# Kernel tuning notes

Hardware: AMD Instinct MI355X
Metric: run time of the kernel (lower is better)

The kernel has to match this reference:

```python
import jax, jax.numpy as jnp
import numpy as np
from jax import lax

N_FRAMES = 256

def _conv(x, w, b):
    # NCHW conv, stride 3 on mel axis (matches MOSNet CNN that collapses mels 81->27->9->3->1)
    y = lax.conv_general_dilated(x, w, window_strides=(1, 3),
                                 padding=((1, 1), (1, 1)),
                                 dimension_numbers=('NCHW', 'OIHW', 'NCHW'))
    return jax.nn.relu(y + b[None, :, None, None])

def _lstm(x, Wih, Whh, bih, bhh, reverse=False):
    # x: [T, B, D] -> hs: [T, B, H]; PyTorch gate order i, f, g, o
    Bsz, H = x.shape[1], Whh.shape[1]
    bias = bih + bhh
    def step(carry, xt):
        h, c = carry
        z = xt @ Wih.T + h @ Whh.T + bias
        i, f, g, o = jnp.split(z, 4, axis=-1)
        c = jax.nn.sigmoid(f) * c + jax.nn.sigmoid(i) * jnp.tanh(g)
        h = jax.nn.sigmoid(o) * jnp.tanh(c)
        return (h, c), h
    init = (jnp.zeros((Bsz, H), x.dtype), jnp.zeros((Bsz, H), x.dtype))
    _, hs = lax.scan(step, init, x, reverse=reverse)
    return hs

def setup_inputs():
    key = jax.random.key(0)
    ks = jax.random.split(key, 24)
    B, T, M = 16, 4096, 81
    chans = [1, 16, 32, 64, 128]
    H = 128
    FC_IN = 2 * H * N_FRAMES  # 65536
    FC_H = 128
    s = 0.05
    inp = {'audio': jax.random.normal(ks[0], (B, T, M), jnp.float32),
           'sample_lengths': jnp.full((B,), T, dtype=jnp.int32)}
    for li in range(4):
        inp['w%d' % li] = jax.random.normal(ks[1 + 2 * li], (chans[li + 1], chans[li], 3, 3), jnp.float32) * s
        inp['b%d' % li] = jnp.zeros((chans[li + 1],), jnp.float32)
    D = chans[-1]
    for d, off in (('f', 9), ('b', 13)):
        inp['Wih_' + d] = jax.random.normal(ks[off], (4 * H, D), jnp.float32) * s
        inp['Whh_' + d] = jax.random.normal(ks[off + 1], (4 * H, H), jnp.float32) * s
        inp['bih_' + d] = jnp.zeros((4 * H,), jnp.float32)
        inp['bhh_' + d] = jnp.zeros((4 * H,), jnp.float32)
    inp['fc1_w'] = jax.random.normal(ks[17], (FC_H, FC_IN), jnp.float32) * 0.005
    inp['fc1_b'] = jnp.zeros((FC_H,), jnp.float32)
    inp['fs_w'] = jax.random.normal(ks[18], (1, FC_H), jnp.float32) * s
    inp['fs_b'] = jnp.zeros((1,), jnp.float32)
    return inp

def reference(audio, w0, b0, w1, b1, w2, b2, w3, b3,
              Wih_f, Whh_f, bih_f, bhh_f, Wih_b, Whh_b, bih_b, bhh_b,
              fc1_w, fc1_b, fs_w, fs_b, sample_lengths):
    B, T, M = audio.shape
    F = T // N_FRAMES  # all lengths == T, multiple of N_FRAMES -> all frames full
    x = audio.reshape(B * F, 1, N_FRAMES, M)   # [BF, 1, nf, mels]
    for w, b in ((w0, b0), (w1, b1), (w2, b2), (w3, b3)):
        x = _conv(x, w, b)                      # mel axis 81->27->9->3->1
    x = x[..., 0].transpose(2, 0, 1)            # [nf, BF, C]
    h_f = _lstm(x, Wih_f, Whh_f, bih_f, bhh_f)
    h_b = _lstm(x, Wih_b, Whh_b, bih_b, bhh_b, reverse=True)
    h = jnp.concatenate([h_f, h_b], axis=-1).transpose(1, 0, 2)  # [BF, nf, 2H]
    flat = h.reshape(B * F, -1)                 # time-major flatten, matches view(1,-1)
    z = jax.nn.relu(flat @ fc1_w.T + fc1_b)     # dropout is identity at inference
    score = jax.nn.sigmoid(z @ fs_w.T + fs_b) * 4.0 + 1.0  # mos range [1,5]
    frames = score.reshape(B, F)
    utt = frames.mean(axis=1)
    return utt, frames
```

## Files before the change

### kernel.cpp

```cpp
#include <hip/hip_runtime.h>
#include <hip/hip_fp16.h>

#define BF 256
#define TSTEPS 256

typedef _Float16 h8_t __attribute__((ext_vector_type(8)));
typedef _Float16 h4_t __attribute__((ext_vector_type(4)));
typedef float f4_t __attribute__((ext_vector_type(4)));

union H8 { uint4 u; h8_t v; };
union H4 { uint2 u; h4_t v; };
union U2H4 { uint2 u; __half h[4]; };

static __device__ __forceinline__ float sigmoidf_(float x) {
    return __builtin_amdgcn_rcpf(1.f + __expf(-x));
}
static __device__ __forceinline__ float tanhf_(float x) {
    return 1.f - 2.f * __builtin_amdgcn_rcpf(__expf(2.f * x) + 1.f);
}

static __device__ __forceinline__ float xswap32(float x, int lane) {
    typedef unsigned uv2 __attribute__((ext_vector_type(2)));
    unsigned xu = __float_as_uint(x);
    uv2 r = __builtin_amdgcn_permlane32_swap(xu, xu, false, false);
    return __uint_as_float((lane & 32) ? r[0] : r[1]);
}

static __device__ __forceinline__ void wg_barrier_lds() {
    __builtin_amdgcn_sched_barrier(0);
    asm volatile("s_waitcnt lgkmcnt(0)" ::: "memory");
    __builtin_amdgcn_s_barrier();
    __builtin_amdgcn_sched_barrier(0);
}

static __device__ __forceinline__ void pack_one(const float* __restrict__ src,
                                                __half* __restrict__ dst,
                                                int OC, int IC, int KS,
                                                int oc_str, int ic_str, int k_str, int i) {
    int grp = KS / 4;
    int j = i % grp;
    int oc = (i / grp) % OC;
    int g = (i / (grp * OC)) & 3;
    int chunk = i / (grp * OC * 4);
    int CPK = IC / KS;
    int cc = chunk % CPK;
    int khw = chunk / CPK;
    int ic = cc * KS + g * grp + j;
    dst[i] = __float2half(src[(long)oc * oc_str + (long)ic * ic_str + khw * k_str]);
}

static __device__ __forceinline__ void pack_whh_one(const float* __restrict__ src,
                                                    __half* __restrict__ dst, int i) {
    int j = i & 7;
    int prow = (i >> 3) & 511;
    int cg = i >> 12;
    int g = cg & 3, chunk = cg >> 2;
    int t = prow >> 4, rr = prow & 15;
    int cls = rr >> 2, du = rr & 3;
    int orig = cls * 128 + t * 4 + du;
    int ic = chunk * 32 + g * 8 + j;
    dst[i] = __float2half(src[orig * 128 + ic]);
}

__global__ __launch_bounds__(256) void prep_k(
        const float* __restrict__ w0, const float* __restrict__ w1,
        const float* __restrict__ w2, const float* __restrict__ w3,
        const float* __restrict__ Wihf, const float* __restrict__ Wihb,
        const float* __restrict__ Whhf, const float* __restrict__ Whhb,
        float* __restrict__ w0t, __half* __restrict__ w1p,
        __half* __restrict__ w2p, __half* __restrict__ w3p,
        __half* __restrict__ wfp, __half* __restrict__ wbp,
        __half* __restrict__ whhfp, __half* __restrict__ whhbp) {
    int i = blockIdx.x * 256 + threadIdx.x;
    if (i < 144) { int oc = i / 9, rem = i % 9; w0t[rem * 16 + oc] = w0[i]; return; }
    i -= 144;
    if (i < 4608) { pack_one(w1, w1p, 32, 16, 16, 144, 9, 1, i); return; }
    i -= 4608;
    if (i < 18432) { pack_one(w2, w2p, 64, 32, 32, 288, 9, 1, i); return; }
    i -= 18432;
    if (i < 73728) { pack_one(w3, w3p, 128, 64, 32, 576, 9, 1, i); return; }
    i -= 73728;
    if (i < 65536) { pack_one(Wihf, wfp, 512, 128, 32, 128, 1, 0, i); return; }
    i -= 65536;
    if (i < 65536) { pack_one(Wihb, wbp, 512, 128, 32, 128, 1, 0, i); return; }
    i -= 65536;
    if (i < 65536) { pack_whh_one(Whhf, whhfp, i); return; }
    i -= 65536;
    if (i < 65536) { pack_whh_one(Whhb, whhbp, i); return; }
}

__global__ void pack_wf16(const float* __restrict__ src, __half* __restrict__ dst,
                          int OC, int IC, int KS,
                          int oc_str, int ic_str, int k_str, int total) {
    int i = blockIdx.x * 256 + threadIdx.x;
    if (i >= total) return;
    pack_one(src, dst, OC, IC, KS, oc_str, ic_str, k_str, i);
}

__global__ __launch_bounds__(256) void conv0_k(const float* __restrict__ in,
                                               const float* __restrict__ wT,
                                               const float* __restrict__ bias,
                                               __half* __restrict__ out) {
    __shared__ float wsm[9][16];
    __shared__ float bs[16];
    int tid = threadIdx.x;
    if (tid < 144) wsm[tid / 16][tid % 16] = wT[tid];
    if (tid < 16) bs[tid] = bias[tid];
    __syncthreads();
    int gid = blockIdx.x * 256 + tid;
    int ow = gid % 27;
    int t = (gid / 27) % 256;
    int bf = gid / (27 * 256);
    float acc[16];
#pragma unroll
    for (int o = 0; o < 16; o++) acc[o] = bs[o];
    int iw0 = ow * 3 - 1;
#pragma unroll
    for (int kh = 0; kh < 3; kh++) {
        int tt = t + kh - 1;
        if ((unsigned)tt >= 256u) continue;
        const float* ip = in + ((long)bf * 256 + tt) * 81;
#pragma unroll
        for (int kw = 0; kw < 3; kw++) {
            int iw = iw0 + kw;
            if ((unsigned)iw >= 81u) continue;
            float x = ip[iw];
#pragma unroll
            for (int o = 0; o < 16; o++) acc[o] += x * wsm[kh * 3 + kw][o];
        }
    }
    union OU { uint4 u; __half2 h2[4]; } o0, o1;
#pragma unroll
    for (int o = 0; o < 4; o++)
        o0.h2[o] = __floats2half2_rn(fmaxf(acc[2 * o], 0.f), fmaxf(acc[2 * o + 1], 0.f));
#pragma unroll
    for (int o = 0; o < 4; o++)
        o1.h2[o] = __floats2half2_rn(fmaxf(acc[8 + 2 * o], 0.f), fmaxf(acc[9 + 2 * o], 0.f));
    uint4* op = (uint4*)(out + (long)gid * 16);
    op[0] = o0.u;
    op[1] = o1.u;
}

template<int IC, int OC, int WIN, int WOUT, int KS>
__global__ __launch_bounds__(256) void convM_k(const __half* __restrict__ in,
                                               const __half* __restrict__ wp,
                                               const float* __restrict__ bias,
                                               __half* __restrict__ out) {
    constexpr int NT = OC / 16;
    constexpr int CPK = IC / KS;
    constexpr int NCHUNK = 9 * CPK;
    constexpr int GRP = KS / 4;
    int tid = threadIdx.x;
    int lane = tid & 63;
    int wv = tid >> 6;
    int l15 = lane & 15;
    int g = lane >> 4;
    int m = blockIdx.x * 64 + wv * 16 + l15;
    int ow = m % WOUT;
    int t = (m / WOUT) % 256;
    int bf = m / (WOUT * 256);

    f4_t acc[NT];
#pragma unroll
    for (int nt = 0; nt < NT; nt++)
#pragma unroll
        for (int r = 0; r < 4; r++) acc[nt][r] = 0.f;

#pragma unroll
    for (int chunk = 0; chunk < NCHUNK; chunk++) {
        int khw = chunk / CPK, cc = chunk % CPK;
        int kh = khw / 3;
        int kw = khw - kh * 3;
        int tt = t + kh - 1;
        int iw = ow * 3 + kw - 1;
        bool ok = ((unsigned)tt < 256u) && ((unsigned)iw < (unsigned)WIN);
        long aoff = ok ? (((long)(bf * 256 + tt) * WIN + iw) * IC + cc * KS + g * GRP) : 0;
        if constexpr (KS == 32) {
            H8 af;
            af.u = *(const uint4*)(in + aoff);
            if (!ok) af.u = make_uint4(0u, 0u, 0u, 0u);
#pragma unroll
            for (int nt = 0; nt < NT; nt++) {
                H8 bf8;
                bf8.u = *(const uint4*)(wp + ((long)(chunk * 4 + g) * OC + nt * 16 + l15) * GRP);
                acc[nt] = __builtin_amdgcn_mfma_f32_16x16x32_f16(af.v, bf8.v, acc[nt], 0, 0, 0);
            }
        } else {
            H4 af;
            af.u = *(const uint2*)(in + aoff);
            if (!ok) af.u = make_uint2(0u, 0u);
#pragma unroll
            for (int nt = 0; nt < NT; nt++) {
                H4 bf4;
                bf4.u = *(const uint2*)(wp + ((long)(chunk * 4 + g) * OC + nt * 16 + l15) * GRP);
                acc[nt] = __builtin_amdgcn_mfma_f32_16x16x16f16(af.v, bf4.v, acc[nt], 0, 0, 0);
            }
        }
    }
    int orow = blockIdx.x * 64 + wv * 16 + g * 4;
#pragma unroll
    for (int nt = 0; nt < NT; nt++) {
        int oc = nt * 16 + l15;
        float b = bias[oc];
#pragma unroll
        for (int r = 0; r < 4; r++) {
            float v = fmaxf(acc[nt][r] + b, 0.f);
            out[(long)(orow + r) * OC + oc] = __float2half(v);
        }
    }
}

__global__ __launch_bounds__(256) void gates_k(const __half* __restrict__ X,
                                               const __half* __restrict__ wpf,
                                               const __half* __restrict__ wpb,
                                               const float* __restrict__ bf1,
                                               const float* __restrict__ bf2,
                                               const float* __restrict__ bb1,
                                               const float* __restrict__ bb2,
                                               __half* __restrict__ Gf,
                                               __half* __restrict__ Gb) {
    int dir = blockIdx.z;
    const __half* wp = dir ? wpb : wpf;
    const float* b1 = dir ? bb1 : bf1;
    const float* b2 = dir ? bb2 : bf2;
    __half* G = dir ? Gb : Gf;
    int tid = threadIdx.x;
    int lane = tid & 63;
    int wv = tid >> 6;
    int l15 = lane & 15;
    int g = lane >> 4;
    int bx = blockIdx.x;
    int b = bx >> 1;
    int t0 = (bx & 1) * 128;
    long r0 = (long)bx * 128 + wv * 32;
    int n0 = blockIdx.y * 128;

    __shared__ __align__(16) __half sh2[128][136];

    f4_t acc[2][8];
#pragma unroll
    for (int s = 0; s < 2; s++)
#pragma unroll
        for (int nt = 0; nt < 8; nt++)
#pragma unroll
            for (int r = 0; r < 4; r++) acc[s][nt][r] = 0.f;

#pragma unroll
    for (int chunk = 0; chunk < 4; chunk++) {
        H8 a0, a1;
        a0.u = *(const uint4*)(X + (r0 + l15) * 128 + chunk * 32 + g * 8);
        a1.u = *(const uint4*)(X + (r0 + 16 + l15) * 128 + chunk * 32 + g * 8);
#pragma unroll
        for (int nt = 0; nt < 8; nt++) {
            H8 bw;
            bw.u = *(const uint4*)(wp + ((long)(chunk * 4 + g) * 512 + n0 + nt * 16 + l15) * 8);
            acc[0][nt] = __builtin_amdgcn_mfma_f32_16x16x32_f16(a0.v, bw.v, acc[0][nt], 0, 0, 0);
            acc[1][nt] = __builtin_amdgcn_mfma_f32_16x16x32_f16(a1.v, bw.v, acc[1][nt], 0, 0, 0);
        }
    }

    int tbw = wv * 32 + g * 4;
#pragma unroll
    for (int nt = 0; nt < 8; nt++) {
        int coll = nt * 16 + l15;
        int col = n0 + coll;
        float bias = b1[col] + b2[col];
#pragma unroll
        for (int s = 0; s < 2; s++) {
            int tbl = tbw + s * 16;
            U2H4 pk;
            if (!dir) {
#pragma unroll
                for (int r = 0; r < 4; r++) pk.h[r] = __float2half(acc[s][nt][r] + bias);
                *(uint2*)&sh2[coll][tbl] = pk.u;
            } else {
#pragma unroll
                for (int r = 0; r < 4; r++) pk.h[3 - r] = __float2half(acc[s][nt][r] + bias);
                *(uint2*)&sh2[coll][124 - tbl] = pk.u;
            }
        }
    }
    __syncthreads();

    int ts_start = dir ? 128 - t0 : t0;
#pragma unroll
    for (int cc = 0; cc < 8; cc++) {
        int idx = cc * 256 + tid;
        int coll = idx >> 4;
        int ch = idx & 15;
        uint4 v = *(const uint4*)&sh2[coll][ch * 8];
        *(uint4*)(G + ((long)(b * 512 + n0 + coll)) * 256 + ts_start + ch * 8) = v;
    }
}

__global__ __launch_bounds__(1024, 4) void lstm_k(const __half* __restrict__ Gf,
                                                  const __half* __restrict__ Gb,
                                                  const __half* __restrict__ whhfp,
                                                  const __half* __restrict__ whhbp,
                                                  __half* __restrict__ flat) {
    int bid = blockIdx.x;
    int dir = bid >> 7;
    int b0 = (bid & 127) * 2;
    const __half* G = dir ? Gb : Gf;
    const __half* wp = dir ? whhbp : whhfp;
    int tid = threadIdx.x;
    int w = tid >> 6;
    int lane = tid & 63;
    int l15 = lane & 15;
    int g2 = lane >> 4;
    int chn = l15 >> 3;
    int u8 = l15 & 7;
    int unit = w * 8 + u8;
    int tsel = (u8 >> 2) & 1;
    int du = u8 & 3;

    H8 afr[2][4];
#pragma unroll
    for (int t = 0; t < 2; t++) {
        int prow = (w * 2 + t) * 16 + l15;
#pragma unroll
        for (int c = 0; c < 4; c++)
            afr[t][c].u = *(const uint4*)(wp + ((long)((c * 4 + g2) * 512 + prow)) * 8);
    }

    __shared__ __align__(16) __half hbuf[2][2][128];
    if (tid < 256) hbuf[0][tid >> 7][tid & 127] = __float2half(0.f);
    __syncthreads();

    const __half* gb0 = G + (((long)(b0 + chn) * 512) + g2 * 128 + unit) * 256;

    float cst = 0.f;
    float ma = (g2 == 2) ? 2.f : 1.f;
    float mb = ma;
    float cb = (g2 == 2) ? -1.f : 0.f;
    const f4_t zero4 = {0.f, 0.f, 0.f, 0.f};

    H8 gc, gn;
    gc.u = *(const uint4*)(gb0);
    long fbase = (long)(b0 + chn) * 65536 + dir * 128 + unit;

    for (int to = 0; to < 32; to++) {
        if (to < 31) gn.u = *(const uint4*)(gb0 + (to + 1) * 8);
#pragma unroll
        for (int ti = 0; ti < 8; ti++) {
            int s = to * 8 + ti;
            int p = s & 1;
            H8 bfr[4];
#pragma unroll
            for (int c = 0; c < 4; c++)
                bfr[c].u = *(const uint4*)(&hbuf[p][chn][c * 32 + g2 * 8]);

            f4_t acc[2];
#pragma unroll
            for (int t = 0; t < 2; t++)
                acc[t] = __builtin_amdgcn_mfma_f32_16x16x32_f16(afr[t][0].v, bfr[0].v,
                                                                zero4, 0, 0, 0);
#pragma unroll
            for (int c = 1; c < 4; c++)
#pragma unroll
                for (int t = 0; t < 2; t++)
                    acc[t] = __builtin_amdgcn_mfma_f32_16x16x32_f16(afr[t][c].v, bfr[c].v,
                                                                    acc[t], 0, 0, 0);
            f4_t at;
#pragma unroll
            for (int e = 0; e < 4; e++) at[e] = tsel ? acc[1][e] : acc[0][e];
            float lo = (du & 1) ? at[1] : at[0];
            float hi = (du & 1) ? at[3] : at[2];
            float ev = (du & 2) ? hi : lo;

            float z = ev + (float)gc.v[ti];
            float a = sigmoidf_(ma * z) * mb + cb;

            float x1 = xswap32(a, lane);
            float pi = a * x1;
            float x2 = __shfl_xor(pi, 16, 64);
            float cn = a * cst + x2;
            cst = cn;
            float tc = tanhf_(cn);
            float x3 = xswap32(tc, lane);
            float h = a * x3;

            if (g2 == 3) {
                __half hh = __float2half(h);
                int ts = dir ? (255 - s) : s;
                hbuf[p ^ 1][chn][unit] = hh;
                flat[fbase + (long)ts * 256] = hh;
            }
            wg_barrier_lds();
        }
        gc = gn;
    }
}

__global__ __launch_bounds__(256) void fc1m_k(const __half* __restrict__ flat,
                                              const __half* __restrict__ wp,
                                              float* __restrict__ z) {
    int tid = threadIdx.x;
    int lane = tid & 63;
    int wv = tid >> 6;
    int l15 = lane & 15;
    int g = lane >> 4;
    int m0 = blockIdx.x * 64 + wv * 16;
    long k0 = (long)blockIdx.y * 1024;

    f4_t acc[8];
#pragma unroll
    for (int nt = 0; nt < 8; nt++)
#pragma unroll
        for (int r = 0; r < 4; r++) acc[nt][r] = 0.f;

    for (int c = 0; c < 32; c++) {
        long chunk = (k0 >> 5) + c;
        H8 af;
        af.u = *(const uint4*)(flat + (long)(m0 + l15) * 65536 + k0 + c * 32 + g * 8);
#pragma unroll
        for (int nt = 0; nt < 8; nt++) {
            H8 bw;
            bw.u = *(const uint4*)(wp + ((chunk * 4 + g) * 128 + nt * 16 + l15) * 8);
            acc[nt] = __builtin_amdgcn_mfma_f32_16x16x32_f16(af.v, bw.v, acc[nt], 0, 0, 0);
        }
    }
#pragma unroll
    for (int nt = 0; nt < 8; nt++)
#pragma unroll
        for (int r = 0; r < 4; r++)
            atomicAdd(&z[(m0 + g * 4 + r) * 128 + nt * 16 + l15], acc[nt][r]);
}

__global__ void zero_k(float* __restrict__ p, int n) {
    int i = blockIdx.x * 256 + threadIdx.x;
    if (i < n) p[i] = 0.f;
}

__global__ __launch_bounds__(256) void head_k(const float* __restrict__ z,
                                              const float* __restrict__ b1,
                                              const float* __restrict__ fsw,
                                              const float* __restrict__ fsb,
                                              float* __restrict__ out) {
    __shared__ float sf[256];
    int r = threadIdx.x;
    float acc = fsb[0];
#pragma unroll
    for (int j4 = 0; j4 < 32; j4++) {
        float4 zv = *(const float4*)&z[r * 128 + j4 * 4];
        float4 bv = *(const float4*)&b1[j4 * 4];
        float4 wv = *(const float4*)&fsw[j4 * 4];
        acc += fmaxf(zv.x + bv.x, 0.f) * wv.x;
        acc += fmaxf(zv.y + bv.y, 0.f) * wv.y;
        acc += fmaxf(zv.z + bv.z, 0.f) * wv.z;
        acc += fmaxf(zv.w + bv.w, 0.f) * wv.w;
    }
    float val = sigmoidf_(acc) * 4.f + 1.f;
    out[16 + r] = val;
    sf[r] = val;
    __syncthreads();
    if (r < 16) {
        float m = 0.f;
#pragma unroll
        for (int f = 0; f < 16; f++) m += sf[r * 16 + f];
        out[r] = m * (1.f / 16.f);
    }
}

extern "C" void kernel_launch(void* const* d_in, const int* in_sizes, int n_in,
                              void* d_out, int out_size, void* d_ws, size_t ws_size,
                              hipStream_t stream) {
    const float* audio = (const float*)d_in[0];
    const float* w0 = (const float*)d_in[2];
    const float* b0 = (const float*)d_in[3];
    const float* w1 = (const float*)d_in[4];
    const float* b1 = (const float*)d_in[5];
    const float* w2 = (const float*)d_in[6];
    const float* b2 = (const float*)d_in[7];
    const float* w3 = (const float*)d_in[8];
    const float* b3 = (const float*)d_in[9];
    const float* Wih_f = (const float*)d_in[10];
    const float* Whh_f = (const float*)d_in[11];
    const float* bih_f = (const float*)d_in[12];
    const float* bhh_f = (const float*)d_in[13];
    const float* Wih_b = (const float*)d_in[14];
    const float* Whh_b = (const float*)d_in[15];
    const float* bih_b = (const float*)d_in[16];
    const float* bhh_b = (const float*)d_in[17];
    const float* fc1_w = (const float*)d_in[18];
    const float* fc1_b = (const float*)d_in[19];
    const float* fs_w = (const float*)d_in[20];
    const float* fs_b = (const float*)d_in[21];
    float* out = (float*)d_out;

    char* ws = (char*)d_ws;
    __half* Gf    = (__half*)(ws);
    __half* out1  = (__half*)(ws);
    __half* fc1p  = (__half*)(ws);
    __half* Gb    = (__half*)(ws + 67108864);
    __half* flat16= (__half*)(ws + 134217728);
    __half* out0  = (__half*)(ws + 134217728);
    __half* X     = (__half*)(ws + 201326592);
    __half* out2  = (__half*)(ws + 218103808);
    char* rd = ws + 243269632;
    float*  w0t   = (float*)(rd);
    __half* w1p   = (__half*)(rd + 1024);
    __half* w2p   = (__half*)(rd + 10240);
    __half* w3p   = (__half*)(rd + 47104);
    __half* wfp   = (__half*)(rd + 194560);
    __half* wbp   = (__half*)(rd + 325632);
    __half* whhfp = (__half*)(rd + 456704);
    __half* whhbp = (__half*)(rd + 587776);
    float*  zbuf  = (float*)(rd + 718848);

    prep_k<<<1403, 256, 0, stream>>>(w0, w1, w2, w3, Wih_f, Wih_b, Whh_f, Whh_b,
                                     w0t, w1p, w2p, w3p, wfp, wbp, whhfp, whhbp);

    conv0_k<<<6912, 256, 0, stream>>>(audio, w0t, b0, out0);
    convM_k<16, 32, 27, 9, 16><<<9216, 256, 0, stream>>>(out0, w1p, b1, out1);
    convM_k<32, 64, 9, 3, 32><<<3072, 256, 0, stream>>>(out1, w2p, b2, out2);
    convM_k<64, 128, 3, 1, 32><<<1024, 256, 0, stream>>>(out2, w3p, b3, X);

    gates_k<<<dim3(512, 4, 2), 256, 0, stream>>>(X, wfp, wbp, bih_f, bhh_f,
                                                 bih_b, bhh_b, Gf, Gb);

    lstm_k<<<256, 1024, 0, stream>>>(Gf, Gb, whhfp, whhbp, flat16);

    pack_wf16<<<32768, 256, 0, stream>>>(fc1_w, fc1p, 128, 65536, 32, 65536, 1, 0, 8388608);
    zero_k<<<128, 256, 0, stream>>>(zbuf, 256 * 128);
    fc1m_k<<<dim3(4, 64), 256, 0, stream>>>(flat16, fc1p, zbuf);
    head_k<<<1, 256, 0, stream>>>(zbuf, fc1_b, fs_w, fs_b, out);
}
```

Baseline: 522.3 us.

## Fuse last conv into gate GEMM and convert fc1 weights inline

The final conv layer and the LSTM input-gate GEMM now run in one kernel. The conv output tile stays in swizzled LDS and feeds the gate MFMAs directly, so the X intermediate never goes to global memory. Separately, the fc1 GEMM reads fp32 weights and converts them to fp16 in registers, which removes the standalone pack kernel and its 16MB write/read. The trade-off is that each fc1 block reads the fp32 weights (twice the bytes), and the fused kernel has heavier per-block register and LDS use.

```diff
diff --git a/kernel.cpp b/kernel.cpp
--- a/kernel.cpp
+++ b/kernel.cpp
@@ -30,6 +30,12 @@
     __builtin_amdgcn_sched_barrier(0);
     asm volatile("s_waitcnt lgkmcnt(0)" ::: "memory");
     __builtin_amdgcn_s_barrier();
+    __builtin_amdgcn_sched_barrier(0);
+}
+
+static __device__ __forceinline__ void wave_lds_fence() {
+    __builtin_amdgcn_sched_barrier(0);
+    asm volatile("s_waitcnt lgkmcnt(0)" ::: "memory");
     __builtin_amdgcn_sched_barrier(0);
 }
 
@@ -89,14 +95,6 @@
     if (i < 65536) { pack_whh_one(Whhb, whhbp, i); return; }
 }
 
-__global__ void pack_wf16(const float* __restrict__ src, __half* __restrict__ dst,
-                          int OC, int IC, int KS,
-                          int oc_str, int ic_str, int k_str, int total) {
-    int i = blockIdx.x * 256 + threadIdx.x;
-    if (i >= total) return;
-    pack_one(src, dst, OC, IC, KS, oc_str, ic_str, k_str, i);
-}
-
 __global__ __launch_bounds__(256) void conv0_k(const float* __restrict__ in,
                                                const float* __restrict__ wT,
                                                const float* __restrict__ bias,
@@ -210,86 +208,150 @@
     }
 }
 
-__global__ __launch_bounds__(256) void gates_k(const __half* __restrict__ X,
-                                               const __half* __restrict__ wpf,
-                                               const __half* __restrict__ wpb,
-                                               const float* __restrict__ bf1,
-                                               const float* __restrict__ bf2,
-                                               const float* __restrict__ bb1,
-                                               const float* __restrict__ bb2,
-                                               __half* __restrict__ Gf,
-                                               __half* __restrict__ Gb) {
-    int dir = blockIdx.z;
-    const __half* wp = dir ? wpb : wpf;
-    const float* b1 = dir ? bb1 : bf1;
-    const float* b2 = dir ? bb2 : bf2;
-    __half* G = dir ? Gb : Gf;
+__global__ __launch_bounds__(256) void c3g_k(const __half* __restrict__ in,
+                                             const __half* __restrict__ wp3,
+                                             const float* __restrict__ bias3,
+                                             const __half* __restrict__ wpf,
+                                             const __half* __restrict__ wpb,
+                                             const float* __restrict__ bf1,
+                                             const float* __restrict__ bf2,
+                                             const float* __restrict__ bb1,
+                                             const float* __restrict__ bb2,
+                                             __half* __restrict__ Gf,
+                                             __half* __restrict__ Gb) {
     int tid = threadIdx.x;
     int lane = tid & 63;
     int wv = tid >> 6;
     int l15 = lane & 15;
     int g = lane >> 4;
-    int bx = blockIdx.x;
-    int b = bx >> 1;
-    int t0 = (bx & 1) * 128;
-    long r0 = (long)bx * 128 + wv * 32;
-    int n0 = blockIdx.y * 128;
-
-    __shared__ __align__(16) __half sh2[128][136];
-
-    f4_t acc[2][8];
-#pragma unroll
-    for (int s = 0; s < 2; s++)
+
+    __shared__ __align__(16) __half Xs[64 * 128];
+    __shared__ __align__(16) __half sh[4][64][72];
+
+    {
+        int m = blockIdx.x * 64 + wv * 16 + l15;
+        int t = m % 256;
+        int bf = m / 256;
+        f4_t acc[8];
 #pragma unroll
         for (int nt = 0; nt < 8; nt++)
 #pragma unroll
-            for (int r = 0; r < 4; r++) acc[s][nt][r] = 0.f;
-
-#pragma unroll
-    for (int chunk = 0; chunk < 4; chunk++) {
-        H8 a0, a1;
-        a0.u = *(const uint4*)(X + (r0 + l15) * 128 + chunk * 32 + g * 8);
-        a1.u = *(const uint4*)(X + (r0 + 16 + l15) * 128 + chunk * 32 + g * 8);
+            for (int r = 0; r < 4; r++) acc[nt][r] = 0.f;
+
+#pragma unroll
+        for (int chunk = 0; chunk < 18; chunk++) {
+            int khw = chunk / 2, cc = chunk % 2;
+            int kh = khw / 3;
+            int kw = khw - kh * 3;
+            int tt = t + kh - 1;
+            int iw = kw - 1;
+            bool ok = ((unsigned)tt < 256u) && ((unsigned)iw < 3u);
+            long aoff = ok ? (((long)(bf * 256 + tt) * 3 + iw) * 64 + cc * 32 + g * 8) : 0;
+            H8 af;
+            af.u = *(const uint4*)(in + aoff);
+            if (!ok) af.u = make_uint4(0u, 0u, 0u, 0u);
+#pragma unroll
+            for (int nt = 0; nt < 8; nt++) {
+                H8 bf8;
+                bf8.u = *(const uint4*)(wp3 + ((long)(chunk * 4 + g) * 128 + nt * 16 + l15) * 8);
+                acc[nt] = __builtin_amdgcn_mfma_f32_16x16x32_f16(af.v, bf8.v, acc[nt], 0, 0, 0);
+            }
+        }
 #pragma unroll
         for (int nt = 0; nt < 8; nt++) {
-            H8 bw;
-            bw.u = *(const uint4*)(wp + ((long)(chunk * 4 + g) * 512 + n0 + nt * 16 + l15) * 8);
-            acc[0][nt] = __builtin_amdgcn_mfma_f32_16x16x32_f16(a0.v, bw.v, acc[0][nt], 0, 0, 0);
-            acc[1][nt] = __builtin_amdgcn_mfma_f32_16x16x32_f16(a1.v, bw.v, acc[1][nt], 0, 0, 0);
-        }
-    }
-
-    int tbw = wv * 32 + g * 4;
-#pragma unroll
-    for (int nt = 0; nt < 8; nt++) {
-        int coll = nt * 16 + l15;
-        int col = n0 + coll;
-        float bias = b1[col] + b2[col];
-#pragma unroll
-        for (int s = 0; s < 2; s++) {
-            int tbl = tbw + s * 16;
-            U2H4 pk;
-            if (!dir) {
-#pragma unroll
-                for (int r = 0; r < 4; r++) pk.h[r] = __float2half(acc[s][nt][r] + bias);
-                *(uint2*)&sh2[coll][tbl] = pk.u;
-            } else {
-#pragma unroll
-                for (int r = 0; r < 4; r++) pk.h[3 - r] = __float2half(acc[s][nt][r] + bias);
-                *(uint2*)&sh2[coll][124 - tbl] = pk.u;
+            int col = nt * 16 + l15;
+            float b = bias3[col];
+#pragma unroll
+            for (int r = 0; r < 4; r++) {
+                int row = wv * 16 + g * 4 + r;
+                float v = fmaxf(acc[nt][r] + b, 0.f);
+                Xs[row * 128 + (col ^ ((row & 7) << 3))] = __float2half(v);
             }
         }
     }
     __syncthreads();
 
-    int ts_start = dir ? 128 - t0 : t0;
-#pragma unroll
-    for (int cc = 0; cc < 8; cc++) {
-        int idx = cc * 256 + tid;
-        int coll = idx >> 4;
-        int ch = idx & 15;
-        uint4 v = *(const uint4*)&sh2[coll][ch * 8];
-        *(uint4*)(G + ((long)(b * 512 + n0 + coll)) * 256 + ts_start + ch * 8) = v;
+    int dir = wv >> 1;
+    int seq = blockIdx.x >> 2;
+    int t0 = (blockIdx.x & 3) * 64;
+    const __half* wpd = dir ? wpb : wpf;
+    const float* bA = dir ? bb1 : bf1;
+    const float* bB = dir ? bb2 : bf2;
+    __half* Gd = dir ? Gb : Gf;
+
+    H8 af2[4][4];
+#pragma unroll
+    for (int rt = 0; rt < 4; rt++) {
+        int row = rt * 16 + l15;
+        int base = row * 128;
+        int sw = (l15 & 7) << 3;
+#pragma unroll
+        for (int c = 0; c < 4; c++)
+            af2[rt][c].u = *(const uint4*)&Xs[base + ((c * 32 + g * 8) ^ sw)];
+    }
+
+    int ts0 = dir ? (192 - t0) : t0;
+#pragma unroll
+    for (int cb = 0; cb < 4; cb++) {
+        int cbase = wv * 256 + cb * 64;
+        f4_t a2[4][4];
+#pragma unroll
+        for (int rt = 0; rt < 4; rt++)
+#pragma unroll
+            for (int ct = 0; ct < 4; ct++)
+#pragma unroll
+                for (int r = 0; r < 4; r++) a2[rt][ct][r] = 0.f;
+
+#pragma unroll
+        for (int c = 0; c < 4; c++) {
+            H8 bw[4];
+#pragma unroll
+            for (int ct = 0; ct < 4; ct++) {
+                int gcol = cbase + ct * 16 + l15 - dir * 512;
+                bw[ct].u = *(const uint4*)(wpd + ((long)((c * 4 + g) * 512 + gcol)) * 8);
+            }
+#pragma unroll
+            for (int rt = 0; rt < 4; rt++)
+#pragma unroll
+                for (int ct = 0; ct < 4; ct++)
+                    a2[rt][ct] = __builtin_amdgcn_mfma_f32_16x16x32_f16(
+                        af2[rt][c].v, bw[ct].v, a2[rt][ct], 0, 0, 0);
+        }
+
+#pragma unroll
+        for (int ct = 0; ct < 4; ct++) {
+            int gcol = cbase + ct * 16 + l15 - dir * 512;
+            float bias = bA[gcol] + bB[gcol];
+            int col_lb = ct * 16 + l15;
+#pragma unroll
+            for (int rt = 0; rt < 4; rt++) {
+                int tl2 = rt * 16 + g * 4;
+#pragma unroll
+                for (int rp = 0; rp < 4; rp += 2) {
+                    __half2 h2;
+                    int pos;
+                    if (!dir) {
+                        h2 = __floats2half2_rn(a2[rt][ct][rp] + bias, a2[rt][ct][rp + 1] + bias);
+                        pos = tl2 + rp;
+                    } else {
+                        h2 = __floats2half2_rn(a2[rt][ct][rp + 1] + bias, a2[rt][ct][rp] + bias);
+                        pos = 62 - (tl2 + rp);
+                    }
+                    *(__half2*)&sh[wv][col_lb][pos] = h2;
+                }
+            }
+        }
+        wave_lds_fence();
+#pragma unroll
+        for (int k = 0; k < 8; k++) {
+            int idx = k * 64 + lane;
+            int col_lb = idx >> 3;
+            int ch = idx & 7;
+            uint4 v = *(const uint4*)&sh[wv][col_lb][ch * 8];
+            int gcol = cbase + col_lb - dir * 512;
+            *(uint4*)(Gd + ((long)(seq * 512 + gcol)) * 256 + ts0 + ch * 8) = v;
+        }
+        wave_lds_fence();
     }
 }
 
@@ -393,7 +455,7 @@
 }
 
 __global__ __launch_bounds__(256) void fc1m_k(const __half* __restrict__ flat,
-                                              const __half* __restrict__ wp,
+                                              const float* __restrict__ fc1w,
                                               float* __restrict__ z) {
     int tid = threadIdx.x;
     int lane = tid & 63;
@@ -410,13 +472,21 @@
         for (int r = 0; r < 4; r++) acc[nt][r] = 0.f;
 
     for (int c = 0; c < 32; c++) {
-        long chunk = (k0 >> 5) + c;
         H8 af;
         af.u = *(const uint4*)(flat + (long)(m0 + l15) * 65536 + k0 + c * 32 + g * 8);
 #pragma unroll
         for (int nt = 0; nt < 8; nt++) {
+            int oc = nt * 16 + l15;
+            const float* wr = fc1w + (long)oc * 65536 + k0 + c * 32 + g * 8;
+            float4 w0v = *(const float4*)(wr);
+            float4 w1v = *(const float4*)(wr + 4);
+            union { uint4 u; __half2 h2[4]; } bwc;
+            bwc.h2[0] = __half2(__float2half(w0v.x), __float2half(w0v.y));
+            bwc.h2[1] = __half2(__float2half(w0v.z), __float2half(w0v.w));
+            bwc.h2[2] = __half2(__float2half(w1v.x), __float2half(w1v.y));
+            bwc.h2[3] = __half2(__float2half(w1v.z), __float2half(w1v.w));
             H8 bw;
-            bw.u = *(const uint4*)(wp + ((chunk * 4 + g) * 128 + nt * 16 + l15) * 8);
+            bw.u = bwc.u;
             acc[nt] = __builtin_amdgcn_mfma_f32_16x16x32_f16(af.v, bw.v, acc[nt], 0, 0, 0);
         }
     }
@@ -491,11 +561,9 @@
     char* ws = (char*)d_ws;
     __half* Gf    = (__half*)(ws);
     __half* out1  = (__half*)(ws);
-    __half* fc1p  = (__half*)(ws);
     __half* Gb    = (__half*)(ws + 67108864);
     __half* flat16= (__half*)(ws + 134217728);
     __half* out0  = (__half*)(ws + 134217728);
-    __half* X     = (__half*)(ws + 201326592);
     __half* out2  = (__half*)(ws + 218103808);
     char* rd = ws + 243269632;
     float*  w0t   = (float*)(rd);
@@ -514,15 +582,13 @@
     conv0_k<<<6912, 256, 0, stream>>>(audio, w0t, b0, out0);
     convM_k<16, 32, 27, 9, 16><<<9216, 256, 0, stream>>>(out0, w1p, b1, out1);
     convM_k<32, 64, 9, 3, 32><<<3072, 256, 0, stream>>>(out1, w2p, b2, out2);
-    convM_k<64, 128, 3, 1, 32><<<1024, 256, 0, stream>>>(out2, w3p, b3, X);
-
-    gates_k<<<dim3(512, 4, 2), 256, 0, stream>>>(X, wfp, wbp, bih_f, bhh_f,
-                                                 bih_b, bhh_b, Gf, Gb);
+
+    c3g_k<<<1024, 256, 0, stream>>>(out2, w3p, b3, wfp, wbp,
+                                    bih_f, bhh_f, bih_b, bhh_b, Gf, Gb);
 
     lstm_k<<<256, 1024, 0, stream>>>(Gf, Gb, whhfp, whhbp, flat16);
 
-    pack_wf16<<<32768, 256, 0, stream>>>(fc1_w, fc1p, 128, 65536, 32, 65536, 1, 0, 8388608);
     zero_k<<<128, 256, 0, stream>>>(zbuf, 256 * 128);
-    fc1m_k<<<dim3(4, 64), 256, 0, stream>>>(flat16, fc1p, zbuf);
+    fc1m_k<<<dim3(4, 64), 256, 0, stream>>>(flat16, fc1_w, zbuf);
     head_k<<<1, 256, 0, stream>>>(zbuf, fc1_b, fs_w, fs_b, out);
 }
```

Result: slower. 597.0 us (+14.3%).
